# Optimization experiments

Measured on AMD Instinct MI355X. Metric: run time of the kernel, lower is better.

## Reference

```python
import jax, jax.numpy as jnp
import numpy as np

N_HEAD, D_EMB, D_MLP, D_HEAD = 12, 768, 3072, 64
LN_EPS = 1e-5


def setup_inputs() -> dict:
    key = jax.random.key(0)
    ks = jax.random.split(key, 12)
    s = 0.02
    return {
        "x": jax.random.normal(ks[0], (2, 4096, D_EMB), dtype=jnp.float32),
        "ln1_g": jnp.ones((D_EMB,), jnp.float32),
        "ln1_b": jnp.zeros((D_EMB,), jnp.float32),
        "wqkv_w": jax.random.normal(ks[1], (D_EMB, 3 * D_EMB), jnp.float32) * s,
        "wo_w": jax.random.normal(ks[2], (D_EMB, D_EMB), jnp.float32) * s,
        "wo_b": jnp.zeros((D_EMB,), jnp.float32),
        "ln2_g": jnp.ones((D_EMB,), jnp.float32),
        "ln2_b": jnp.zeros((D_EMB,), jnp.float32),
        "w1_w": jax.random.normal(ks[3], (D_EMB, D_MLP), jnp.float32) * s,
        "w1_b": jnp.zeros((D_MLP,), jnp.float32),
        "w2_w": jax.random.normal(ks[4], (D_MLP, D_EMB), jnp.float32) * s,
        "w2_b": jnp.zeros((D_EMB,), jnp.float32),
    }


def _layernorm(x, g, b):
    mu = jnp.mean(x, axis=-1, keepdims=True)
    var = jnp.var(x, axis=-1, keepdims=True)
    return (x - mu) * jax.lax.rsqrt(var + LN_EPS) * g + b


def _attn(x, wqkv_w, wo_w, wo_b):
    B, T, d = x.shape
    qkv = x @ wqkv_w  # [B,T,3d]
    q, k, v = jnp.split(qkv, 3, axis=-1)
    q = q.reshape(B, T, N_HEAD, D_HEAD).transpose(0, 2, 1, 3)  # [B,H,T,dh]
    k = k.reshape(B, T, N_HEAD, D_HEAD).transpose(0, 2, 1, 3)
    v = v.reshape(B, T, N_HEAD, D_HEAD).transpose(0, 2, 1, 3)
    A = jnp.einsum('bhqd,bhkd->bhqk', q, k) / np.sqrt(D_HEAD).astype(np.float32)
    mask = jnp.tril(jnp.ones((T, T), dtype=bool))
    A = jnp.where(mask, A, -jnp.inf)
    A = jax.nn.softmax(A - jax.lax.stop_gradient(jnp.max(A, axis=-1, keepdims=True)), axis=-1)
    y = jnp.einsum('bhqk,bhkd->bhqd', A, v)  # [B,H,T,dh]
    y = y.transpose(0, 2, 1, 3).reshape(B, T, d)
    return y @ wo_w + wo_b


def _mlp(x, w1_w, w1_b, w2_w, w2_b):
    h = jax.nn.gelu(x @ w1_w + w1_b, approximate=False)
    return h @ w2_w + w2_b


def reference(x, ln1_g, ln1_b, wqkv_w, wo_w, wo_b, ln2_g, ln2_b, w1_w, w1_b, w2_w, w2_b):
    x = x + _attn(_layernorm(x, ln1_g, ln1_b), wqkv_w, wo_w, wo_b)
    x = x + _mlp(_layernorm(x, ln2_g, ln2_b), w1_w, w1_b, w2_w, w2_b)
    return x
```

## Files before the change

kernel.cpp:

```cpp
#include <hip/hip_runtime.h>

#define T_SEQ 4096
#define D_EMB 768
#define N_HEAD 12
#define D_HEAD 64
#define D_MLP 3072
#define NTOK 8192
#define QSCALE 0.18033688011112043f

typedef __bf16 v8bf __attribute__((ext_vector_type(8)));
typedef float v4f __attribute__((ext_vector_type(4)));
typedef short v4s __attribute__((ext_vector_type(4)));
typedef unsigned v2u __attribute__((ext_vector_type(2)));

template <int N> struct IC { static constexpr int value = N; };

__device__ __forceinline__ unsigned short f2bf(float f) {
    unsigned int u = __float_as_uint(f);
    unsigned int r = (u + 0x7fffu + ((u >> 16) & 1u)) >> 16;
    return (unsigned short)r;
}

__device__ __forceinline__ void g2lds16(const void* g, void* l) {
    __builtin_amdgcn_global_load_lds(
        (const __attribute__((address_space(1))) void*)g,
        (__attribute__((address_space(3))) void*)l, 16, 0, 0);
}

__device__ __forceinline__ float fastrcp(float x) {
#if __has_builtin(__builtin_amdgcn_rcpf)
    return __builtin_amdgcn_rcpf(x);
#else
    return 1.f / x;
#endif
}

__device__ __forceinline__ void pl32swap(unsigned& a, unsigned& b) {
#if __has_builtin(__builtin_amdgcn_permlane32_swap)
    v2u r = __builtin_amdgcn_permlane32_swap(a, b, false, false);
    a = r[0]; b = r[1];
#else
    asm volatile("v_permlane32_swap_b32 %0, %1" : "+v"(a), "+v"(b));
#endif
}
__device__ __forceinline__ void pl16swap(unsigned& a, unsigned& b) {
#if __has_builtin(__builtin_amdgcn_permlane16_swap)
    v2u r = __builtin_amdgcn_permlane16_swap(a, b, false, false);
    a = r[0]; b = r[1];
#else
    asm volatile("v_permlane16_swap_b32 %0, %1" : "+v"(a), "+v"(b));
#endif
}

__device__ __forceinline__ int sg(int r) { return (r ^ (r >> 2)) & 3; }

__global__ void tcast_kernel(const float* __restrict__ in, unsigned short* __restrict__ out,
                             int K, int N) {
    __shared__ float tile[32][33];
    int k0 = blockIdx.y * 32, n0 = blockIdx.x * 32;
    int tx = threadIdx.x, ty = threadIdx.y;
    for (int i = ty; i < 32; i += 8)
        tile[i][tx] = in[(size_t)(k0 + i) * N + n0 + tx];
    __syncthreads();
    for (int i = ty; i < 32; i += 8)
        out[(size_t)(n0 + i) * K + k0 + tx] = f2bf(tile[tx][i]);
}

__global__ void vtrans_kernel(const unsigned short* __restrict__ in,
                              unsigned short* __restrict__ out) {
    __shared__ unsigned short tile[32][33];
    size_t base = (size_t)blockIdx.z * T_SEQ * D_HEAD;
    int t0 = blockIdx.x * 32, d0 = blockIdx.y * 32;
    int tx = threadIdx.x, ty = threadIdx.y;
    for (int i = ty; i < 32; i += 8)
        tile[i][tx] = in[base + (size_t)(t0 + i) * D_HEAD + d0 + tx];
    __syncthreads();
    size_t tbase = base + (size_t)(t0 >> 6) * 4096 + (t0 & 32);
    for (int i = ty; i < 32; i += 8)
        out[tbase + (size_t)(d0 + i) * 64 + tx] = tile[tx][i];
}

__global__ __launch_bounds__(256) void ln_kernel(const float* __restrict__ x,
                                                 const float* __restrict__ g,
                                                 const float* __restrict__ bta,
                                                 unsigned short* __restrict__ out) {
    int row = blockIdx.x;
    const float* xr = x + (size_t)row * D_EMB;
    int tid = threadIdx.x;
    float v[3];
    float s = 0.f, s2 = 0.f;
#pragma unroll
    for (int i = 0; i < 3; i++) {
        v[i] = xr[tid + i * 256];
        s += v[i];
        s2 += v[i] * v[i];
    }
#pragma unroll
    for (int o = 1; o < 64; o <<= 1) {
        s += __shfl_xor(s, o);
        s2 += __shfl_xor(s2, o);
    }
    __shared__ float red[8];
    int wave = tid >> 6, lane = tid & 63;
    if (lane == 0) { red[wave] = s; red[wave + 4] = s2; }
    __syncthreads();
    s = red[0] + red[1] + red[2] + red[3];
    s2 = red[4] + red[5] + red[6] + red[7];
    float mu = s * (1.f / 768.f);
    float var = s2 * (1.f / 768.f) - mu * mu;
    float rstd = rsqrtf(var + 1e-5f);
#pragma unroll
    for (int i = 0; i < 3; i++) {
        int c = tid + i * 256;
        out[(size_t)row * D_EMB + c] = f2bf((v[i] - mu) * rstd * g[c] + bta[c]);
    }
}

template <int EPI, int MT>
__global__ __launch_bounds__(256) void gemm_kernel(
    const unsigned short* __restrict__ A, const unsigned short* __restrict__ Bt, int K,
    int Nt, const float* __restrict__ bias, const float* __restrict__ resid,
    float* __restrict__ outF, unsigned short* __restrict__ outB,
    unsigned short* __restrict__ Qb, unsigned short* __restrict__ Kb,
    unsigned short* __restrict__ Vb) {
    constexpr int NAI = (MT == 128) ? 4 : 2;
    __shared__ unsigned short As[3][MT * 32];
    __shared__ unsigned short Bs[3][4096];
    const int tid = threadIdx.x;
    const int wave = tid >> 6, lane = tid & 63;
    const int n16 = lane & 15, kq = lane >> 4;
    const int moff = (wave >> 1) * (MT / 2), noff = (wave & 1) * 64;
    const int id = blockIdx.x;
    const int xcd = id & 7, s = id >> 3;
    const int mt = xcd * (NTOK / MT / 8) + s / Nt, nt_ = s % Nt;
    const long m0 = (long)mt * MT, nb0 = (long)nt_ * 128;

    const int c0 = (wave * 2 + 0) * 64 + lane;
    const int c1 = (wave * 2 + 1) * 64 + lane;
    const int r0 = c0 >> 2, r1 = c1 >> 2;
    const unsigned short* bP0 = Bt + (nb0 + r0) * K + (((c0 & 3) ^ sg(r0)) << 3);
    const unsigned short* bP1 = Bt + (nb0 + r1) * K + (((c1 & 3) ^ sg(r1)) << 3);
    const int ca = (MT == 128) ? c0 : (wave * 64 + lane);
    const int ra = ca >> 2;
    const unsigned short* aP0 = A + (m0 + ra) * K + (((ca & 3) ^ sg(ra)) << 3);
    const unsigned short* aP1 = (MT == 128)
        ? A + (m0 + r1) * K + (((c1 & 3) ^ sg(r1)) << 3) : nullptr;
    const int sn = sg(n16);
    const int fw = (noff + n16) * 32 + ((kq ^ sn) << 3);
    const int fa = (moff + n16) * 32 + ((kq ^ sn) << 3);

    const v4f vzero = {0.f, 0.f, 0.f, 0.f};
    v4f acc[4][NAI];
#pragma unroll
    for (int wi = 0; wi < 4; wi++)
#pragma unroll
        for (int ai = 0; ai < NAI; ai++) acc[wi][ai] = vzero;

    auto stage = [&](int nb, int kpos) {
        unsigned short* asb = &As[0][0] + nb * (MT * 32);
        unsigned short* bsb = &Bs[0][0] + nb * 4096;
        if (MT == 128) {
            g2lds16(aP0 + kpos, asb + (wave * 2 + 0) * 512);
            g2lds16(aP1 + kpos, asb + (wave * 2 + 1) * 512);
        } else {
            g2lds16(aP0 + kpos, asb + wave * 512);
        }
        g2lds16(bP0 + kpos, bsb + (wave * 2 + 0) * 512);
        g2lds16(bP1 + kpos, bsb + (wave * 2 + 1) * 512);
    };
    auto waitL = [&]() {
        if constexpr (MT == 128) {
            asm volatile("s_waitcnt vmcnt(4)" ::: "memory");
        } else {
            asm volatile("s_waitcnt vmcnt(3)" ::: "memory");
        }
        __builtin_amdgcn_s_barrier();
        __builtin_amdgcn_sched_barrier(0);
    };
    auto wait0 = [&]() {
        asm volatile("s_waitcnt vmcnt(0)" ::: "memory");
        __builtin_amdgcn_s_barrier();
        __builtin_amdgcn_sched_barrier(0);
    };
    auto compute = [&](int nb) {
        const unsigned short* asb = &As[0][0] + nb * (MT * 32);
        const unsigned short* bsb = &Bs[0][0] + nb * 4096;
        v8bf wf[4], af[NAI];
#pragma unroll
        for (int i = 0; i < 4; i++) wf[i] = *(const v8bf*)(bsb + fw + i * 512);
#pragma unroll
        for (int i = 0; i < NAI; i++) af[i] = *(const v8bf*)(asb + fa + i * 512);
#pragma unroll
        for (int wi = 0; wi < 4; wi++)
#pragma unroll
            for (int ai = 0; ai < NAI; ai++)
                acc[wi][ai] = __builtin_amdgcn_mfma_f32_16x16x32_bf16(wf[wi], af[ai],
                                                                     acc[wi][ai], 0, 0, 0);
    };

    stage(0, 0);
    stage(1, 32);
    const int nsteps = K / 32;
    int b0 = 0;
#pragma unroll 1
    for (int i = 0; i < nsteps - 2; i++) {
        waitL();
        int b2 = b0 + 2; if (b2 >= 3) b2 -= 3;
        stage(b2, (i + 2) * 32);
        compute(b0);
        b0++; if (b0 >= 3) b0 = 0;
    }
    waitL();
    compute(b0);
    b0++; if (b0 >= 3) b0 = 0;
    wait0();
    compute(b0);

#pragma unroll
    for (int wi = 0; wi < 4; wi++) {
#pragma unroll
        for (int ai = 0; ai < NAI; ai++) {
            const long Nb = nb0 + noff + wi * 16 + kq * 4;
            const long M = m0 + moff + ai * 16 + n16;
            if (EPI == 0) {
                int which = (int)(Nb / 768);
                int c = (int)(Nb - which * 768);
                int hh = c >> 6, ii = c & 63;
                int bb = (int)(M >> 12), t = (int)(M & 4095);
                size_t dst = (((size_t)bb * N_HEAD + hh) * T_SEQ + t) * D_HEAD + ii;
                union { uint2 u2; unsigned short us[4]; } pk;
#pragma unroll
                for (int r = 0; r < 4; r++) {
                    float v = acc[wi][ai][r];
                    if (which == 0) v *= QSCALE;
                    pk.us[r] = f2bf(v);
                }
                if (which == 0) *(uint2*)(&Qb[dst]) = pk.u2;
                else if (which == 1) *(uint2*)(&Kb[dst]) = pk.u2;
                else *(uint2*)(&Vb[dst]) = pk.u2;
            } else if (EPI == 1) {
                float4 b4 = *(const float4*)(&bias[Nb]);
                float4 r4 = *(const float4*)(&resid[M * 768 + Nb]);
                float4 o4;
                o4.x = acc[wi][ai][0] + b4.x + r4.x;
                o4.y = acc[wi][ai][1] + b4.y + r4.y;
                o4.z = acc[wi][ai][2] + b4.z + r4.z;
                o4.w = acc[wi][ai][3] + b4.w + r4.w;
                *(float4*)(&outF[M * 768 + Nb]) = o4;
            } else {
                float4 b4 = *(const float4*)(&bias[Nb]);
                union { uint2 u2; unsigned short us[4]; } pk;
#pragma unroll
                for (int r = 0; r < 4; r++) {
                    float t = acc[wi][ai][r] + ((const float*)&b4)[r];
                    float y = t * (-2.302118131f + t * t * -0.1029433585f);
                    float gl = t * fastrcp(1.f + __builtin_amdgcn_exp2f(y));
                    pk.us[r] = f2bf(gl);
                }
                *(uint2*)(&outB[M * 3072 + Nb]) = pk.u2;
            }
        }
    }
}

__global__ __launch_bounds__(256) void attn_kernel(const unsigned short* __restrict__ Q,
                                                   const unsigned short* __restrict__ Kg,
                                                   const unsigned short* __restrict__ Vt,
                                                   unsigned short* __restrict__ y) {
    __shared__ unsigned short Kt[2][4096];
    __shared__ unsigned short Vl[2][4096];
    const int tid = threadIdx.x;
    const int wave = tid >> 6, lane = tid & 63;
    const int n16 = lane & 15, kq = lane >> 4;
    const int id = blockIdx.x;
    const int xcd = id & 7, slot = id >> 3;
    const int combo = xcd * 3 + (slot % 3);
    const int qt = 63 - slot / 3;
    const int h = combo % N_HEAD, b = combo / N_HEAD;
    const size_t hoff = (((size_t)b * N_HEAD + h) * T_SEQ) * D_HEAD;
    const unsigned short* Qh = Q + hoff;
    const unsigned short* Kh = Kg + hoff;
    const unsigned short* Vh = Vt + hoff;
    const v4f vzero = {0.f, 0.f, 0.f, 0.f};

    const int sC0 = (wave * 2 + 0) * 64 + lane;
    const int sC1 = (wave * 2 + 1) * 64 + lane;
    const int soff0 = (sC0 >> 3) * 64 + ((((sC0 & 7) ^ ((sC0 >> 3) & 7))) << 3);
    const int soff1 = (sC1 >> 3) * 64 + ((((sC1 & 7) ^ ((sC1 >> 3) & 7))) << 3);
    const int fb0 = n16 * 64 + ((kq ^ (n16 & 7)) << 3);
    const int fb1 = n16 * 64 + (((4 + kq) ^ (n16 & 7)) << 3);
    v8bf vone;
#pragma unroll
    for (int j = 0; j < 8; j++) ((unsigned short*)&vone)[j] = 0x3F80;

    const int qglob = qt * 64 + wave * 16 + n16;
    v8bf qf[2];
#pragma unroll
    for (int ks = 0; ks < 2; ks++)
        qf[ks] = *(const v8bf*)(&Qh[(size_t)qglob * D_HEAD + ks * 32 + kq * 8]);

    v4f o[4], lacc;
#pragma unroll
    for (int nt = 0; nt < 4; nt++) o[nt] = vzero;
    lacc = vzero;

    const unsigned short* knext;
    const unsigned short* vnext;

    auto step = [&](auto BUFC, int kt, bool pref, bool diag) {
        constexpr int buf = decltype(BUFC)::value;
        __syncthreads();
        if (pref) {
            g2lds16(knext + soff0, &Kt[buf ^ 1][(wave * 2 + 0) * 512]);
            g2lds16(knext + soff1, &Kt[buf ^ 1][(wave * 2 + 1) * 512]);
            g2lds16(vnext + soff0, &Vl[buf ^ 1][(wave * 2 + 0) * 512]);
            g2lds16(vnext + soff1, &Vl[buf ^ 1][(wave * 2 + 1) * 512]);
            knext += 4096;
            vnext += 4096;
        }
        v4f s[4];
#pragma unroll
        for (int nt = 0; nt < 4; nt++) s[nt] = vzero;
        __builtin_amdgcn_s_setprio(1);
#pragma unroll
        for (int nt = 0; nt < 4; nt++) {
            v8bf k0 = *(const v8bf*)(&Kt[buf][nt * 1024 + fb0]);
            v8bf k1 = *(const v8bf*)(&Kt[buf][nt * 1024 + fb1]);
            s[nt] = __builtin_amdgcn_mfma_f32_16x16x32_bf16(k0, qf[0], s[nt], 0, 0, 0);
            s[nt] = __builtin_amdgcn_mfma_f32_16x16x32_bf16(k1, qf[1], s[nt], 0, 0, 0);
        }
        __builtin_amdgcn_s_setprio(0);
        union PW { v4s s4; unsigned u[2]; } pa[4];
#pragma unroll
        for (int ntk = 0; ntk < 4; ntk++) {
            union { v4s s4; __bf16 h[4]; } pk;
#pragma unroll
            for (int r = 0; r < 4; r++) {
                float p = __builtin_amdgcn_exp2f(s[ntk][r]);
                if (diag) {
                    int key = kt * 64 + ntk * 16 + kq * 4 + r;
                    if (key > qglob) p = 0.f;
                }
                pk.h[r] = (__bf16)p;
            }
            pa[ntk].s4 = pk.s4;
        }
        union F8 { v8bf v; unsigned u[4]; } pf[2];
#pragma unroll
        for (int ks = 0; ks < 2; ks++) {
#pragma unroll
            for (int j = 0; j < 2; j++) {
                unsigned X = pa[2 * ks].u[j], Y = pa[2 * ks + 1].u[j];
                pl32swap(X, Y);
                pl16swap(X, Y);
                pf[ks].u[j] = X;
                pf[ks].u[j + 2] = Y;
            }
        }
        __builtin_amdgcn_s_setprio(1);
#pragma unroll
        for (int ks = 0; ks < 2; ks++) {
            lacc = __builtin_amdgcn_mfma_f32_16x16x32_bf16(pf[ks].v, vone, lacc, 0, 0, 0);
#pragma unroll
            for (int nt = 0; nt < 4; nt++) {
                v8bf vb = *(const v8bf*)(&Vl[buf][nt * 1024 + (ks ? fb1 : fb0)]);
                o[nt] = __builtin_amdgcn_mfma_f32_16x16x32_bf16(pf[ks].v, vb, o[nt], 0, 0, 0);
            }
        }
        __builtin_amdgcn_s_setprio(0);
    };

    g2lds16(Kh + soff0, &Kt[0][(wave * 2 + 0) * 512]);
    g2lds16(Kh + soff1, &Kt[0][(wave * 2 + 1) * 512]);
    g2lds16(Vh + soff0, &Vl[0][(wave * 2 + 0) * 512]);
    g2lds16(Vh + soff1, &Vl[0][(wave * 2 + 1) * 512]);
    knext = Kh + 4096;
    vnext = Vh + 4096;

    int kt = 0;
#pragma unroll 1
    while (kt + 2 <= qt) {
        step(IC<0>{}, kt, true, false);
        step(IC<1>{}, kt + 1, true, false);
        kt += 2;
    }
    if (kt < qt) {
        step(IC<0>{}, kt, true, false);
        step(IC<1>{}, kt + 1, false, true);
    } else {
        step(IC<0>{}, kt, false, true);
    }

    float linv[4];
#pragma unroll
    for (int r = 0; r < 4; r++) linv[r] = fastrcp(lacc[r]);
#pragma unroll
    for (int nt = 0; nt < 4; nt++)
#pragma unroll
        for (int r = 0; r < 4; r++) {
            int q = qt * 64 + wave * 16 + kq * 4 + r;
            float val = o[nt][r] * linv[r];
            y[((size_t)b * T_SEQ + q) * D_EMB + h * 64 + nt * 16 + n16] = f2bf(val);
        }
}

extern "C" void kernel_launch(void* const* d_in, const int* in_sizes, int n_in,
                              void* d_out, int out_size, void* d_ws, size_t ws_size,
                              hipStream_t stream) {
    const float* x = (const float*)d_in[0];
    const float* ln1_g = (const float*)d_in[1];
    const float* ln1_b = (const float*)d_in[2];
    const float* wqkv_w = (const float*)d_in[3];
    const float* wo_w = (const float*)d_in[4];
    const float* wo_b = (const float*)d_in[5];
    const float* ln2_g = (const float*)d_in[6];
    const float* ln2_b = (const float*)d_in[7];
    const float* w1_w = (const float*)d_in[8];
    const float* w1_b = (const float*)d_in[9];
    const float* w2_w = (const float*)d_in[10];
    const float* w2_b = (const float*)d_in[11];
    float* out = (float*)d_out;

    char* ws = (char*)d_ws;
    size_t off = 0;
    auto alloc = [&](size_t bytes) -> void* {
        void* p = ws + off;
        off += (bytes + 255) & ~(size_t)255;
        return p;
    };
    unsigned short* xn = (unsigned short*)alloc((size_t)NTOK * D_EMB * 2);
    unsigned short* wqkvT = (unsigned short*)alloc((size_t)2304 * 768 * 2);
    unsigned short* woT = (unsigned short*)alloc((size_t)768 * 768 * 2);
    unsigned short* w1T = (unsigned short*)alloc((size_t)3072 * 768 * 2);
    unsigned short* w2T = (unsigned short*)alloc((size_t)768 * 3072 * 2);
    unsigned short* Qb = (unsigned short*)alloc((size_t)NTOK * D_EMB * 2);
    unsigned short* Kb = (unsigned short*)alloc((size_t)NTOK * D_EMB * 2);
    unsigned short* Vb = (unsigned short*)alloc((size_t)NTOK * D_EMB * 2);
    unsigned short* yb = (unsigned short*)alloc((size_t)NTOK * D_EMB * 2);
    float* res1 = (float*)alloc((size_t)NTOK * D_EMB * 4);
    unsigned short* Vtb = xn;
    unsigned short* hbuf = Qb;

    dim3 tb(32, 8);
    tcast_kernel<<<dim3(2304 / 32, 768 / 32), tb, 0, stream>>>(wqkv_w, wqkvT, 768, 2304);
    tcast_kernel<<<dim3(768 / 32, 768 / 32), tb, 0, stream>>>(wo_w, woT, 768, 768);
    tcast_kernel<<<dim3(3072 / 32, 768 / 32), tb, 0, stream>>>(w1_w, w1T, 768, 3072);
    tcast_kernel<<<dim3(768 / 32, 3072 / 32), tb, 0, stream>>>(w2_w, w2T, 3072, 768);

    ln_kernel<<<NTOK, 256, 0, stream>>>(x, ln1_g, ln1_b, xn);

    gemm_kernel<0, 128><<<1152, 256, 0, stream>>>(
        xn, wqkvT, 768, 18, nullptr, nullptr, nullptr, nullptr, Qb, Kb, Vb);

    vtrans_kernel<<<dim3(T_SEQ / 32, 2, 2 * N_HEAD), tb, 0, stream>>>(Vb, Vtb);

    attn_kernel<<<1536, 256, 0, stream>>>(Qb, Kb, Vtb, yb);

    gemm_kernel<1, 64><<<768, 256, 0, stream>>>(
        yb, woT, 768, 6, wo_b, x, res1, nullptr, nullptr, nullptr, nullptr);

    ln_kernel<<<NTOK, 256, 0, stream>>>(res1, ln2_g, ln2_b, xn);

    gemm_kernel<2, 128><<<1536, 256, 0, stream>>>(
        xn, w1T, 768, 24, w1_b, nullptr, nullptr, hbuf, nullptr, nullptr, nullptr);

    gemm_kernel<1, 64><<<768, 256, 0, stream>>>(
        hbuf, w2T, 3072, 6, w2_b, res1, out, nullptr, nullptr, nullptr, nullptr);
}
```

Baseline: 424.7 us.

## Split GEMM pipelining: double-buffer for wide GEMMs, 4-stage for output projections

Adds a PIPE template flag to the GEMM. The QKV and W1 GEMMs switch from a 3-buffer vmcnt-based pipeline to a simpler 2-buffer loop with __syncthreads. The Wo and W2 GEMMs switch from 64-row tiles to 128-row tiles with a 4-buffer prefetch pipeline that keeps three stages in flight, halving their grid to 384 blocks. The aim is less LDS use and higher occupancy for the large GEMMs, and more latency hiding and reuse for the narrow ones, at the cost of fewer blocks on the N=768 GEMMs.

```diff
diff --git a/kernel.cpp b/kernel.cpp
--- a/kernel.cpp
+++ b/kernel.cpp
@@ -116,7 +116,7 @@
     }
 }
 
-template <int EPI, int MT>
+template <int EPI, int MT, bool PIPE>
 __global__ __launch_bounds__(256) void gemm_kernel(
     const unsigned short* __restrict__ A, const unsigned short* __restrict__ Bt, int K,
     int Nt, const float* __restrict__ bias, const float* __restrict__ resid,
@@ -124,8 +124,9 @@
     unsigned short* __restrict__ Qb, unsigned short* __restrict__ Kb,
     unsigned short* __restrict__ Vb) {
     constexpr int NAI = (MT == 128) ? 4 : 2;
-    __shared__ unsigned short As[3][MT * 32];
-    __shared__ unsigned short Bs[3][4096];
+    constexpr int NBUF = PIPE ? 4 : 2;
+    __shared__ unsigned short As[NBUF][MT * 32];
+    __shared__ unsigned short Bs[NBUF][4096];
     const int tid = threadIdx.x;
     const int wave = tid >> 6, lane = tid & 63;
     const int n16 = lane & 15, kq = lane >> 4;
@@ -168,20 +169,6 @@
         g2lds16(bP0 + kpos, bsb + (wave * 2 + 0) * 512);
         g2lds16(bP1 + kpos, bsb + (wave * 2 + 1) * 512);
     };
-    auto waitL = [&]() {
-        if constexpr (MT == 128) {
-            asm volatile("s_waitcnt vmcnt(4)" ::: "memory");
-        } else {
-            asm volatile("s_waitcnt vmcnt(3)" ::: "memory");
-        }
-        __builtin_amdgcn_s_barrier();
-        __builtin_amdgcn_sched_barrier(0);
-    };
-    auto wait0 = [&]() {
-        asm volatile("s_waitcnt vmcnt(0)" ::: "memory");
-        __builtin_amdgcn_s_barrier();
-        __builtin_amdgcn_sched_barrier(0);
-    };
     auto compute = [&](int nb) {
         const unsigned short* asb = &As[0][0] + nb * (MT * 32);
         const unsigned short* bsb = &Bs[0][0] + nb * 4096;
@@ -198,23 +185,43 @@
                                                                      acc[wi][ai], 0, 0, 0);
     };
 
-    stage(0, 0);
-    stage(1, 32);
-    const int nsteps = K / 32;
-    int b0 = 0;
+    if constexpr (PIPE) {
+        stage(0, 0);
+        stage(1, 32);
+        stage(2, 64);
+        const int nsteps = K / 32;
 #pragma unroll 1
-    for (int i = 0; i < nsteps - 2; i++) {
-        waitL();
-        int b2 = b0 + 2; if (b2 >= 3) b2 -= 3;
-        stage(b2, (i + 2) * 32);
-        compute(b0);
-        b0++; if (b0 >= 3) b0 = 0;
-    }
-    waitL();
-    compute(b0);
-    b0++; if (b0 >= 3) b0 = 0;
-    wait0();
-    compute(b0);
+        for (int i = 0; i < nsteps - 3; i++) {
+            asm volatile("s_waitcnt vmcnt(8)" ::: "memory");
+            __builtin_amdgcn_s_barrier();
+            __builtin_amdgcn_sched_barrier(0);
+            stage((i + 3) & 3, (i + 3) * 32);
+            compute(i & 3);
+        }
+        asm volatile("s_waitcnt vmcnt(8)" ::: "memory");
+        __builtin_amdgcn_s_barrier();
+        __builtin_amdgcn_sched_barrier(0);
+        compute((nsteps - 3) & 3);
+        asm volatile("s_waitcnt vmcnt(4)" ::: "memory");
+        __builtin_amdgcn_s_barrier();
+        __builtin_amdgcn_sched_barrier(0);
+        compute((nsteps - 2) & 3);
+        asm volatile("s_waitcnt vmcnt(0)" ::: "memory");
+        __builtin_amdgcn_s_barrier();
+        __builtin_amdgcn_sched_barrier(0);
+        compute((nsteps - 1) & 3);
+    } else {
+        stage(0, 0);
+#pragma unroll 1
+        for (int k0 = 0; k0 < K; k0 += 64) {
+            __syncthreads();
+            stage(1, k0 + 32);
+            compute(0);
+            __syncthreads();
+            if (k0 + 64 < K) stage(0, k0 + 64);
+            compute(1);
+        }
+    }
 
 #pragma unroll
     for (int wi = 0; wi < 4; wi++) {
@@ -449,21 +456,21 @@
 
     ln_kernel<<<NTOK, 256, 0, stream>>>(x, ln1_g, ln1_b, xn);
 
-    gemm_kernel<0, 128><<<1152, 256, 0, stream>>>(
+    gemm_kernel<0, 128, false><<<1152, 256, 0, stream>>>(
         xn, wqkvT, 768, 18, nullptr, nullptr, nullptr, nullptr, Qb, Kb, Vb);
 
     vtrans_kernel<<<dim3(T_SEQ / 32, 2, 2 * N_HEAD), tb, 0, stream>>>(Vb, Vtb);
 
     attn_kernel<<<1536, 256, 0, stream>>>(Qb, Kb, Vtb, yb);
 
-    gemm_kernel<1, 64><<<768, 256, 0, stream>>>(
+    gemm_kernel<1, 128, true><<<384, 256, 0, stream>>>(
         yb, woT, 768, 6, wo_b, x, res1, nullptr, nullptr, nullptr, nullptr);
 
     ln_kernel<<<NTOK, 256, 0, stream>>>(res1, ln2_g, ln2_b, xn);
 
-    gemm_kernel<2, 128><<<1536, 256, 0, stream>>>(
+    gemm_kernel<2, 128, false><<<1536, 256, 0, stream>>>(
         xn, w1T, 768, 24, w1_b, nullptr, nullptr, hbuf, nullptr, nullptr, nullptr);
 
-    gemm_kernel<1, 64><<<768, 256, 0, stream>>>(
+    gemm_kernel<1, 128, true><<<384, 256, 0, stream>>>(
         hbuf, w2T, 3072, 6, w2_b, res1, out, nullptr, nullptr, nullptr, nullptr);
 }
```

Result: slower. 472.9 us (+11.4%).
